# Kernel optimization log

Measured on AMD Instinct MI355X. Metric: run time of the kernel, lower is better.

Reference implementation:

```python
import jax, jax.numpy as jnp
import numpy as np

EMBED = 512
HEADS = 8
FMUL = 4
TAU = 2.0
V_TH = 1.0      # spiking threshold (spikingjelly default)
ALPHA = 2.0     # ATan surrogate alpha (spikingjelly default)
EPS = 1e-5


@jax.custom_vjp
def spike_fn(v):
    # Heaviside spike with ATan surrogate gradient (spikingjelly surrogate.ATan)
    return (v >= V_TH).astype(v.dtype)

def _spike_fwd(v):
    return spike_fn(v), v

def _spike_bwd(v, g):
    t = (jnp.pi / 2.0) * ALPHA * (v - V_TH)
    return (g * (ALPHA / 2.0) / (1.0 + t * t),)

spike_fn.defvjp(_spike_fwd, _spike_bwd)


def layernorm(x, g, b):
    mu = jnp.mean(x, axis=-1, keepdims=True)
    var = jnp.mean(jnp.square(x - mu), axis=-1, keepdims=True)
    return (x - mu) * jax.lax.rsqrt(var + EPS) * g + b


def setup_inputs() -> dict:
    key = jax.random.key(0)
    ks = jax.random.split(key, 12)
    m, s, e = 4, 2048, EMBED
    f = e * FMUL
    sc = 0.02
    return {
        "x":  jax.random.normal(ks[0], (m, s, e), jnp.float32),
        "wq": jax.random.normal(ks[1], (e, e), jnp.float32) * sc,
        "bq": jnp.zeros((e,), jnp.float32),
        "wk": jax.random.normal(ks[2], (e, e), jnp.float32) * sc,
        "bk": jnp.zeros((e,), jnp.float32),
        "wv": jax.random.normal(ks[3], (e, e), jnp.float32) * sc,
        "bv": jnp.zeros((e,), jnp.float32),
        "w1": jax.random.normal(ks[4], (e, f), jnp.float32) * sc,
        "b1": jnp.zeros((f,), jnp.float32),
        "w2": jax.random.normal(ks[5], (f, e), jnp.float32) * sc,
        "b2": jnp.zeros((e,), jnp.float32),
        "g1": jnp.ones((e,), jnp.float32),
        "be1": jnp.zeros((e,), jnp.float32),
        "g2": jnp.ones((e,), jnp.float32),
        "be2": jnp.zeros((e,), jnp.float32),
    }


def reference(x, wq, bq, wk, bk, wv, bv, w1, b1, w2, b2, g1, be1, g2, be2):
    m, s, e = x.shape
    h = HEADS
    d = e // h

    # --- pre-norm attention (NOTE: original has NO 1/sqrt(d) scaling) ---
    n1 = layernorm(x, g1, be1)
    q = (n1 @ wq + bq).reshape(m, s, h, d).transpose(0, 2, 1, 3)  # [m,h,s,d]
    k = (n1 @ wk + bk).reshape(m, s, h, d).transpose(0, 2, 1, 3)
    v = (n1 @ wv + bv).reshape(m, s, h, d).transpose(0, 2, 1, 3)
    scores = jnp.einsum('bhqd,bhkd->bhqk', q, k)       # [m,h,s,s], unscaled
    attn = jax.nn.softmax(scores, axis=-1)
    ctx = jnp.einsum('bhqk,bhkd->bhqd', attn, v)       # [m,h,s,d]
    att_out = ctx.transpose(0, 2, 1, 3).reshape(m, s, e)

    x = x + att_out
    # dropout p=0.4 is identity at inference (eval path in the original)

    # --- FFN with spiking activation ---
    n2 = layernorm(x, g2, be2)
    h1 = n2 @ w1 + b1                                  # [m,s,4e]
    # single-step LIF charge from v=0: v = v + (x - v)/tau = x/tau
    spikes = spike_fn(h1 / TAU)
    return x + (spikes @ w2 + b2)
```

## Files before the change

kernel.cpp:

```cpp
#include <hip/hip_runtime.h>
#include <stdint.h>

#define EMB 512
#define SEQ 2048
#define MB 4
#define NH 8
#define HD 64
#define ROWS (MB*SEQ)
#define MARGIN 0.02f
#define CAP 65536
#define LOG2E 1.44269504f
#define EXPB (-17.3123405f)

typedef unsigned short u16;
typedef __attribute__((ext_vector_type(8))) short bf16x8;
typedef __attribute__((ext_vector_type(4))) float f32x4;
typedef __attribute__((ext_vector_type(2))) unsigned int u32x2;
typedef __attribute__((ext_vector_type(4))) unsigned int u32x4;

union Frag { u32x2 u[2]; bf16x8 v; };
union Frag4 { unsigned u[4]; bf16x8 v; };

__device__ __forceinline__ u16 f2bf(float f) {
  union { float f; unsigned u; } a; a.f = f;
  unsigned r = a.u + 0x7FFFu + ((a.u >> 16) & 1u);
  return (u16)(r >> 16);
}
__device__ __forceinline__ float bflo(unsigned u) {
  union { unsigned u; float f; } c; c.u = u << 16; return c.f;
}
__device__ __forceinline__ float bfhi(unsigned u) {
  union { unsigned u; float f; } c; c.u = u & 0xffff0000u; return c.f;
}
__device__ __forceinline__ void gld16(const void* g, void* l) {
  __builtin_amdgcn_global_load_lds(
      (const __attribute__((address_space(1))) void*)g,
      (__attribute__((address_space(3))) void*)l, 16, 0, 0);
}


__global__ __launch_bounds__(256) void k_prep(
    const float* __restrict__ x, const float* __restrict__ g1, const float* __restrict__ be1,
    const float* __restrict__ wq, const float* __restrict__ wk,
    const float* __restrict__ wv, const float* __restrict__ w1,
    u16* __restrict__ n1, u16* __restrict__ wqkvT, u16* __restrict__ w1T,
    int* __restrict__ cnt) {
  __shared__ float tile[32][33];
  int b = blockIdx.x, tid = threadIdx.x;
  if (b < 1792) {
    const float* src; u16* dst; int N, bx, by;
    if (b < 768) {
      int z = b >> 8, rem = b & 255; bx = rem & 15; by = rem >> 4; N = 512;
      src = (z == 0) ? wq : ((z == 1) ? wk : wv);
      dst = wqkvT + z * 512 * 512;
    } else {
      int rem = b - 768; bx = rem & 63; by = rem >> 6; N = 2048;
      src = w1; dst = w1T;
    }
    int tx = tid & 31, ty = tid >> 5;
    int k0 = by * 32, n0 = bx * 32;
    for (int i = 0; i < 32; i += 8)
      tile[ty + i][tx] = src[(size_t)(k0 + ty + i) * N + n0 + tx];
    __syncthreads();
    for (int i = 0; i < 32; i += 8)
      dst[(size_t)(n0 + ty + i) * 512 + k0 + tx] = f2bf(tile[tx][ty + i]);
  } else {
    if (b == 1792 && tid < 2) cnt[tid] = 0;
    int wid = tid >> 6, lane = tid & 63;
    int row = (b - 1792) * 4 + wid;
    const float* xr = x + (size_t)row * EMB + lane * 8;
    f32x4 v0 = *(const f32x4*)xr;
    f32x4 v1 = *(const f32x4*)(xr + 4);
    float s = v0.x+v0.y+v0.z+v0.w + v1.x+v1.y+v1.z+v1.w;
    float q = v0.x*v0.x+v0.y*v0.y+v0.z*v0.z+v0.w*v0.w
            + v1.x*v1.x+v1.y*v1.y+v1.z*v1.z+v1.w*v1.w;
    #pragma unroll
    for (int o = 1; o < 64; o <<= 1) { s += __shfl_xor(s, o); q += __shfl_xor(q, o); }
    float mu = s * (1.0f/512.0f);
    float rs = 1.0f / sqrtf(q * (1.0f/512.0f) - mu*mu + 1e-5f);
    f32x4 ga = *(const f32x4*)(g1 + lane*8), gb = *(const f32x4*)(g1 + lane*8 + 4);
    f32x4 ba = *(const f32x4*)(be1 + lane*8), bb = *(const f32x4*)(be1 + lane*8 + 4);
    union { u16 h[8]; u32x4 v; } o8;
    o8.h[0] = f2bf((v0.x-mu)*rs*ga.x + ba.x); o8.h[1] = f2bf((v0.y-mu)*rs*ga.y + ba.y);
    o8.h[2] = f2bf((v0.z-mu)*rs*ga.z + ba.z); o8.h[3] = f2bf((v0.w-mu)*rs*ga.w + ba.w);
    o8.h[4] = f2bf((v1.x-mu)*rs*gb.x + bb.x); o8.h[5] = f2bf((v1.y-mu)*rs*gb.y + bb.y);
    o8.h[6] = f2bf((v1.z-mu)*rs*gb.z + bb.z); o8.h[7] = f2bf((v1.w-mu)*rs*gb.w + bb.w);
    *(u32x4*)(n1 + (size_t)row * EMB + lane * 8) = o8.v;
  }
}

__global__ __launch_bounds__(256) void k_ln2(const float* __restrict__ x,
    const u16* __restrict__ att, const float* __restrict__ g, const float* __restrict__ b,
    const float* __restrict__ b2, float* __restrict__ x2, u16* __restrict__ n2,
    float* __restrict__ out) {
  int wid = threadIdx.x >> 6, lane = threadIdx.x & 63;
  int row = blockIdx.x * 4 + wid;
  size_t base = (size_t)row * EMB + lane * 8;
  u32x4 av = *(const u32x4*)(att + base);
  f32x4 t0, t1;
  t0.x = bflo(av.x); t0.y = bfhi(av.x); t0.z = bflo(av.y); t0.w = bfhi(av.y);
  t1.x = bflo(av.z); t1.y = bfhi(av.z); t1.z = bflo(av.w); t1.w = bfhi(av.w);
  f32x4 v0 = *(const f32x4*)(x + base)     + t0;
  f32x4 v1 = *(const f32x4*)(x + base + 4) + t1;
  *(f32x4*)(x2 + base) = v0;
  *(f32x4*)(x2 + base + 4) = v1;
  *(f32x4*)(out + base)     = v0 + *(const f32x4*)(b2 + lane*8);
  *(f32x4*)(out + base + 4) = v1 + *(const f32x4*)(b2 + lane*8 + 4);
  float s = v0.x+v0.y+v0.z+v0.w + v1.x+v1.y+v1.z+v1.w;
  float q = v0.x*v0.x+v0.y*v0.y+v0.z*v0.z+v0.w*v0.w
          + v1.x*v1.x+v1.y*v1.y+v1.z*v1.z+v1.w*v1.w;
  #pragma unroll
  for (int o = 1; o < 64; o <<= 1) { s += __shfl_xor(s, o); q += __shfl_xor(q, o); }
  float mu = s * (1.0f/512.0f);
  float rs = 1.0f / sqrtf(q * (1.0f/512.0f) - mu*mu + 1e-5f);
  f32x4 ga = *(const f32x4*)(g + lane*8), gb = *(const f32x4*)(g + lane*8 + 4);
  f32x4 ba = *(const f32x4*)(b + lane*8), bb = *(const f32x4*)(b + lane*8 + 4);
  union { u16 h[8]; u32x4 v; } o8;
  o8.h[0] = f2bf((v0.x-mu)*rs*ga.x + ba.x); o8.h[1] = f2bf((v0.y-mu)*rs*ga.y + ba.y);
  o8.h[2] = f2bf((v0.z-mu)*rs*ga.z + ba.z); o8.h[3] = f2bf((v0.w-mu)*rs*ga.w + ba.w);
  o8.h[4] = f2bf((v1.x-mu)*rs*gb.x + bb.x); o8.h[5] = f2bf((v1.y-mu)*rs*gb.y + bb.y);
  o8.h[6] = f2bf((v1.z-mu)*rs*gb.z + bb.z); o8.h[7] = f2bf((v1.w-mu)*rs*gb.w + bb.w);
  *(u32x4*)(n2 + (size_t)row * EMB + lane * 8) = o8.v;
}

#define GEMM_CORE(A_, Bt_, m0_, n0_)                                           \
  __shared__ u16 As[2][128 * 32];                                              \
  __shared__ u16 Bs[2][128 * 32];                                              \
  int tid = threadIdx.x;                                                       \
  int wid = tid >> 6, lane = tid & 63;                                         \
  int quad = lane >> 4, ln15 = lane & 15;                                      \
  int wm = (wid >> 1) * 64, wn = (wid & 1) * 64;                               \
  int arow = lane >> 2, acol = (lane & 3) * 8;                                 \
  const u16* gA0 = A_  + (size_t)(m0_ + wid * 32 + arow) * 512 + acol;         \
  const u16* gA1 = gA0 + (size_t)16 * 512;                                     \
  const u16* gB0 = Bt_ + (size_t)(n0_ + wid * 32 + arow) * 512 + acol;         \
  const u16* gB1 = gB0 + (size_t)16 * 512;                                     \
  f32x4 acc[4][4] = {};                                                        \
  gld16(gA0, &As[0][(wid * 32) * 32]); gld16(gA1, &As[0][(wid * 32 + 16) * 32]);\
  gld16(gB0, &Bs[0][(wid * 32) * 32]); gld16(gB1, &Bs[0][(wid * 32 + 16) * 32]);\
  for (int kt = 0; kt < 16; kt++) {                                            \
    int cur = kt & 1;                                                          \
    __syncthreads();                                                           \
    if (kt < 15) {                                                             \
      int ko = (kt + 1) * 32;                                                  \
      gld16(gA0 + ko, &As[cur ^ 1][(wid * 32) * 32]);                          \
      gld16(gA1 + ko, &As[cur ^ 1][(wid * 32 + 16) * 32]);                     \
      gld16(gB0 + ko, &Bs[cur ^ 1][(wid * 32) * 32]);                          \
      gld16(gB1 + ko, &Bs[cur ^ 1][(wid * 32 + 16) * 32]);                     \
    }                                                                          \
    bf16x8 af[4], bf[4];                                                       \
    _Pragma("unroll")                                                          \
    for (int i = 0; i < 4; i++) {                                              \
      af[i] = *(const bf16x8*)&As[cur][(wm + i * 16 + ln15) * 32 + quad * 8];  \
      bf[i] = *(const bf16x8*)&Bs[cur][(wn + i * 16 + ln15) * 32 + quad * 8];  \
    }                                                                          \
    _Pragma("unroll")                                                          \
    for (int i = 0; i < 4; i++)                                                \
      _Pragma("unroll")                                                        \
      for (int j = 0; j < 4; j++)                                              \
        acc[i][j] = __builtin_amdgcn_mfma_f32_16x16x32_bf16(af[i], bf[j],      \
                                                            acc[i][j], 0, 0, 0);\
  }                                                                            \
  __syncthreads();

__global__ __launch_bounds__(256) void k_gemm_qkv(
    const u16* __restrict__ A, const u16* __restrict__ Bt,
    const float* __restrict__ bq, const float* __restrict__ bk, const float* __restrict__ bv,
    u16* __restrict__ Qb, u16* __restrict__ Kb, u16* __restrict__ Vtb) {
  int m0 = blockIdx.y * 128, n0 = blockIdx.x * 128;
  GEMM_CORE(A, Bt, m0, n0)
  #pragma unroll
  for (int j = 0; j < 4; j++) {
    int n = n0 + wn + j * 16 + ln15;
    int t = n >> 9, cc = n & 511, head = cc >> 6, dd = cc & 63;
    float bias = (t == 0) ? bq[cc] : ((t == 1) ? bk[cc] : bv[cc]);
    #pragma unroll
    for (int i = 0; i < 4; i++) {
      int row0 = m0 + wm + i * 16 + quad * 4;
      int mm = row0 >> 11, ss0 = row0 & 2047;
      if (t == 2) {
        union { u16 h[4]; u32x2 v; } pk;
        #pragma unroll
        for (int r = 0; r < 4; r++) pk.h[r] = f2bf(acc[i][j][r] + bias);
        *(u32x2*)(Vtb + ((size_t)(mm * 8 + head) * 64 + dd) * 2048 + ss0) = pk.v;
      } else {
        u16* dst = (t == 0) ? Qb : Kb;
        #pragma unroll
        for (int r = 0; r < 4; r++)
          dst[((size_t)(mm * 8 + head) * 2048 + ss0 + r) * 64 + dd] =
              f2bf(acc[i][j][r] + bias);
      }
    }
  }
}

__global__ __launch_bounds__(256) void k_gemm_ffn1(
    const u16* __restrict__ A, const u16* __restrict__ Bt, const float* __restrict__ b1,
    int* __restrict__ cnt, unsigned* __restrict__ spikeL, unsigned* __restrict__ candL) {
  int m0 = blockIdx.y * 128, n0 = blockIdx.x * 128;
  GEMM_CORE(A, Bt, m0, n0)
  #pragma unroll
  for (int j = 0; j < 4; j++) {
    int n = n0 + wn + j * 16 + ln15;
    float bias = b1[n];
    #pragma unroll
    for (int i = 0; i < 4; i++) {
      #pragma unroll
      for (int r = 0; r < 4; r++) {
        int row = m0 + wm + i * 16 + quad * 4 + r;
        float hv = acc[i][j][r] + bias;
        if (hv >= 2.0f - MARGIN) {
          if (hv >= 2.0f + MARGIN) {
            int ix = atomicAdd(&cnt[0], 1);
            if (ix < CAP) spikeL[ix] = (unsigned)(row * 2048 + n);
          } else {
            int ix = atomicAdd(&cnt[1], 1);
            if (ix < CAP) candL[ix] = (unsigned)(row * 2048 + n);
          }
        }
      }
    }
  }
}

#define F_STAGE(BUF, T0)                                                       \
  do {                                                                         \
    gld16(gK0 + (size_t)(T0)       * 4096, &L.SB[BUF][0][0][rb0 * 64]);        \
    gld16(gK1 + (size_t)(T0)       * 4096, &L.SB[BUF][0][0][rb1 * 64]);        \
    gld16(gK0 + (size_t)((T0) + 1) * 4096, &L.SB[BUF][0][1][rb0 * 64]);        \
    gld16(gK1 + (size_t)((T0) + 1) * 4096, &L.SB[BUF][0][1][rb1 * 64]);        \
    gld16(gV0 + (T0) * 64,       &L.SB[BUF][1][0][rb0 * 64]);                  \
    gld16(gV1 + (T0) * 64,       &L.SB[BUF][1][0][rb1 * 64]);                  \
    gld16(gV0 + ((T0) + 1) * 64, &L.SB[BUF][1][1][rb0 * 64]);                  \
    gld16(gV1 + ((T0) + 1) * 64, &L.SB[BUF][1][1][rb1 * 64]);                  \
  } while (0)

#define F_INNER(BUF, SUB)                                                      \
  do {                                                                         \
    const u16* Kc = L.SB[BUF][0][SUB];                                         \
    const u16* Vc = L.SB[BUF][1][SUB];                                         \
    f32x4 s4[2][4];                                                            \
    _Pragma("unroll")                                                          \
    for (int j = 0; j < 4; j++) {                                              \
      bf16x8 a = *(const bf16x8*)(Kc + (j * 16 + ln15) * 64 + ((quad ^ lm) * 8)); \
      s4[0][j] = __builtin_amdgcn_mfma_f32_16x16x32_bf16(a, aQ[0][0].v, z4, 0, 0, 0); \
      s4[1][j] = __builtin_amdgcn_mfma_f32_16x16x32_bf16(a, aQ[1][0].v, z4, 0, 0, 0); \
    }                                                                          \
    _Pragma("unroll")                                                          \
    for (int j = 0; j < 4; j++) {                                              \
      bf16x8 a = *(const bf16x8*)(Kc + (j * 16 + ln15) * 64 + (((4 + quad) ^ lm) * 8)); \
      s4[0][j] = __builtin_amdgcn_mfma_f32_16x16x32_bf16(a, aQ[0][1].v, s4[0][j], 0, 0, 0); \
      s4[1][j] = __builtin_amdgcn_mfma_f32_16x16x32_bf16(a, aQ[1][1].v, s4[1][j], 0, 0, 0); \
    }                                                                          \
    Frag4 bP[2][2];                                                            \
    _Pragma("unroll")                                                          \
    for (int h = 0; h < 2; h++) {                                              \
      unsigned pr[4][4];                                                       \
      _Pragma("unroll")                                                        \
      for (int j = 0; j < 4; j++)                                              \
        _Pragma("unroll")                                                      \
        for (int r = 0; r < 4; r++) {                                          \
          float p = __builtin_amdgcn_exp2f(fmaf(s4[h][j][r], LOG2E, EXPB));    \
          l[h] += p;                                                           \
          union { float f; unsigned u; } cc; cc.f = p;                         \
          pr[j][r] = cc.u;                                                     \
        }                                                                      \
      _Pragma("unroll")                                                        \
      for (int t = 0; t < 2; t++) {                                            \
        bP[h][t].u[0] = __builtin_amdgcn_perm(pr[2*t][1],   pr[2*t][0],   0x07060302u); \
        bP[h][t].u[1] = __builtin_amdgcn_perm(pr[2*t][3],   pr[2*t][2],   0x07060302u); \
        bP[h][t].u[2] = __builtin_amdgcn_perm(pr[2*t+1][1], pr[2*t+1][0], 0x07060302u); \
        bP[h][t].u[3] = __builtin_amdgcn_perm(pr[2*t+1][3], pr[2*t+1][2], 0x07060302u); \
      }                                                                        \
    }                                                                          \
    _Pragma("unroll")                                                          \
    for (int t = 0; t < 2; t++)                                                \
      _Pragma("unroll")                                                        \
      for (int j = 0; j < 4; j++) {                                            \
        int row = j * 16 + ln15;                                               \
        int c0 = 4 * t + (quad >> 1), sub = (quad & 1) * 4;                    \
        Frag aV;                                                               \
        aV.u[0] = *(const u32x2*)(Vc + row * 64 + ((c0 ^ lm) * 8) + sub);      \
        aV.u[1] = *(const u32x2*)(Vc + row * 64 + (((c0 + 2) ^ lm) * 8) + sub);\
        U[0][j] = __builtin_amdgcn_mfma_f32_16x16x32_bf16(aV.v, bP[0][t].v,    \
                                                          U[0][j], 0, 0, 0);   \
        U[1][j] = __builtin_amdgcn_mfma_f32_16x16x32_bf16(aV.v, bP[1][t].v,    \
                                                          U[1][j], 0, 0, 0);   \
      }                                                                        \
  } while (0)

#define F_STEP(CUR, S)                                                         \
  do {                                                                         \
    __syncthreads();                                                           \
    if ((S) < 15) F_STAGE((CUR) ^ 1, 2 * (S) + 2);                             \
    F_INNER(CUR, 0);                                                           \
    F_INNER(CUR, 1);                                                           \
  } while (0)

__global__ __launch_bounds__(256, 2) void k_flash(
    const u16* __restrict__ Q, const u16* __restrict__ K,
    const u16* __restrict__ Vt, u16* __restrict__ att) {
  __shared__ union {
    u16 SB[2][2][2][64 * 64];
    float T[4][16 * 68];
  } L;
  int tid = threadIdx.x, wid = tid >> 6, lane = tid & 63;
  int quad = lane >> 4, ln15 = lane & 15, lm = ln15 & 7;
  int qb = blockIdx.x, head = blockIdx.y, mm = blockIdx.z;
  int mh = mm * 8 + head;
  const u16* Qp = Q  + (size_t)mh * SEQ * HD;
  const u16* Kp = K  + (size_t)mh * SEQ * HD;
  const u16* Vp = Vt + (size_t)mh * HD * SEQ;
  int q0 = qb * 128 + wid * 32;

  Frag aQ[2][2];
  #pragma unroll
  for (int h = 0; h < 2; h++)
    #pragma unroll
    for (int t = 0; t < 2; t++) {
      u32x4 g = *(const u32x4*)(Qp + (size_t)(q0 + h * 16 + ln15) * 64 + t * 32 + quad * 8);
      aQ[h][t].u[0].x = g.x; aQ[h][t].u[0].y = g.y;
      aQ[h][t].u[1].x = g.z; aQ[h][t].u[1].y = g.w;
    }
  const f32x4 z4 = {0.f, 0.f, 0.f, 0.f};

  int srow = lane >> 3;
  int sch  = (lane & 7) ^ (srow & 7);
  int rb0 = wid * 16, rb1 = wid * 16 + 8;
  const u16* gK0 = Kp + (size_t)(rb0 + srow) * 64 + sch * 8;
  const u16* gK1 = Kp + (size_t)(rb1 + srow) * 64 + sch * 8;
  const u16* gV0 = Vp + (size_t)(rb0 + srow) * SEQ + sch * 8;
  const u16* gV1 = Vp + (size_t)(rb1 + srow) * SEQ + sch * 8;

  float l[2] = {0.f, 0.f};
  f32x4 U[2][4] = {};

  F_STAGE(0, 0);
  for (int it = 0; it < 8; it++) {
    F_STEP(0, 2 * it);
    F_STEP(1, 2 * it + 1);
  }
  __syncthreads();

  #pragma unroll
  for (int h = 0; h < 2; h++) {
    float lv = l[h];
    lv += __shfl_xor(lv, 16);
    lv += __shfl_xor(lv, 32);
    float rl = 1.0f / lv;
    float* Tw = L.T[wid];
    #pragma unroll
    for (int j = 0; j < 4; j++)
      *(f32x4*)(Tw + ln15 * 68 + j * 16 + quad * 4) = U[h][j] * rl;
    #pragma unroll
    for (int s = 0; s < 4; s++) {
      f32x4 o = *(const f32x4*)(Tw + (quad * 4 + s) * 68 + ln15 * 4);
      union { u16 h4[4]; u32x2 v; } pk;
      pk.h4[0] = f2bf(o.x); pk.h4[1] = f2bf(o.y);
      pk.h4[2] = f2bf(o.z); pk.h4[3] = f2bf(o.w);
      *(u32x2*)(att + ((size_t)mm * SEQ + q0 + h * 16 + quad * 4 + s) * EMB +
                head * 64 + ln15 * 4) = pk.v;
    }
  }
}

__global__ __launch_bounds__(256) void k_fixup(
    const float* __restrict__ x2, const float* __restrict__ w1, const float* __restrict__ b1,
    const float* __restrict__ g2, const float* __restrict__ be2,
    int* __restrict__ cnt, unsigned* __restrict__ spikeL, const unsigned* __restrict__ candL) {
  __shared__ float sb[8];
  int tid = threadIdx.x;
  int nC = cnt[1]; if (nC > CAP) nC = CAP;
  for (int e = blockIdx.x; e < nC; e += gridDim.x) {
    unsigned v = candL[e];
    int row = (int)(v >> 11), col = (int)(v & 2047u);
    const float* xr = x2 + (size_t)row * 512;
    float x0 = xr[tid], x1 = xr[tid + 256];
    float s = x0 + x1, q = x0 * x0 + x1 * x1;
    #pragma unroll
    for (int o = 1; o < 64; o <<= 1) { s += __shfl_xor(s, o); q += __shfl_xor(q, o); }
    if ((tid & 63) == 0) { sb[tid >> 6] = s; sb[4 + (tid >> 6)] = q; }
    __syncthreads();
    float st = sb[0] + sb[1] + sb[2] + sb[3];
    float qt = sb[4] + sb[5] + sb[6] + sb[7];
    __syncthreads();
    float mu = st * (1.f / 512.f);
    float rs = 1.f / sqrtf(qt * (1.f / 512.f) - mu * mu + 1e-5f);
    float na = (x0 - mu) * rs * g2[tid] + be2[tid];
    float nb = (x1 - mu) * rs * g2[tid + 256] + be2[tid + 256];
    float dd = na * w1[(size_t)tid * 2048 + col] + nb * w1[(size_t)(tid + 256) * 2048 + col];
    #pragma unroll
    for (int o = 1; o < 64; o <<= 1) dd += __shfl_xor(dd, o);
    if ((tid & 63) == 0) sb[tid >> 6] = dd;
    __syncthreads();
    if (tid == 0) {
      float hv = sb[0] + sb[1] + sb[2] + sb[3] + b1[col];
      if (hv >= 2.0f) { int ix = atomicAdd(&cnt[0], 1); if (ix < CAP) spikeL[ix] = v; }
    }
    __syncthreads();
  }
}

__global__ void k_apply(const float* __restrict__ w2, const int* __restrict__ cnt,
                        const unsigned* __restrict__ spikeL, float* __restrict__ out) {
  int n = cnt[0]; if (n > CAP) n = CAP;
  int tid = threadIdx.x;
  for (int e = blockIdx.x; e < n; e += gridDim.x) {
    unsigned v = spikeL[e];
    int row = (int)(v >> 11), col = (int)(v & 2047u);
    atomicAdd(&out[(size_t)row * 512 + tid * 2 + 0], w2[(size_t)col * 512 + tid * 2 + 0]);
    atomicAdd(&out[(size_t)row * 512 + tid * 2 + 1], w2[(size_t)col * 512 + tid * 2 + 1]);
  }
}


extern "C" void kernel_launch(void* const* d_in, const int* in_sizes, int n_in,
                              void* d_out, int out_size, void* d_ws, size_t ws_size,
                              hipStream_t stream) {
  (void)in_sizes; (void)n_in; (void)out_size; (void)ws_size;
  const float* x   = (const float*)d_in[0];
  const float* wq  = (const float*)d_in[1];
  const float* bq  = (const float*)d_in[2];
  const float* wk  = (const float*)d_in[3];
  const float* bk  = (const float*)d_in[4];
  const float* wv  = (const float*)d_in[5];
  const float* bv  = (const float*)d_in[6];
  const float* w1  = (const float*)d_in[7];
  const float* b1  = (const float*)d_in[8];
  const float* w2  = (const float*)d_in[9];
  const float* b2  = (const float*)d_in[10];
  const float* g1  = (const float*)d_in[11];
  const float* be1 = (const float*)d_in[12];
  const float* g2  = (const float*)d_in[13];
  const float* be2 = (const float*)d_in[14];
  float* out = (float*)d_out;

  char* w = (char*)d_ws;
  size_t off = 0;
  auto take = [&](size_t bytes) { char* p = w + off; off += (bytes + 255) & ~(size_t)255; return p; };
  int*      cnt    = (int*)take(256);
  u16*      n1     = (u16*)take((size_t)ROWS * EMB * 2);
  u16*      wqkvT  = (u16*)take((size_t)1536 * 512 * 2);
  u16*      w1T    = (u16*)take((size_t)2048 * 512 * 2);
  u16*      Qb     = (u16*)take((size_t)MB * NH * SEQ * HD * 2);
  u16*      Kb     = (u16*)take((size_t)MB * NH * SEQ * HD * 2);
  u16*      Vtb    = (u16*)take((size_t)MB * NH * SEQ * HD * 2);
  u16*      att    = (u16*)take((size_t)ROWS * EMB * 2);
  float*    x2     = (float*)take((size_t)ROWS * EMB * 4);
  u16*      n2     = (u16*)take((size_t)ROWS * EMB * 2);
  unsigned* spikeL = (unsigned*)take((size_t)CAP * 4);
  unsigned* candL  = (unsigned*)take((size_t)CAP * 4);

  k_prep<<<3840, 256, 0, stream>>>(x, g1, be1, wq, wk, wv, w1, n1, wqkvT, w1T, cnt);
  k_gemm_qkv<<<dim3(12, 64), 256, 0, stream>>>(n1, wqkvT, bq, bk, bv, Qb, Kb, Vtb);
  k_flash<<<dim3(16, 8, 4), 256, 0, stream>>>(Qb, Kb, Vtb, att);
  k_ln2<<<ROWS / 4, 256, 0, stream>>>(x, att, g2, be2, b2, x2, n2, out);
  k_gemm_ffn1<<<dim3(16, 64), 256, 0, stream>>>(n2, w1T, b1, cnt, spikeL, candL);
  k_fixup<<<256, 256, 0, stream>>>(x2, w1, b1, g2, be2, cnt, spikeL, candL);
  k_apply<<<128, 256, 0, stream>>>(w2, cnt, spikeL, out);
}
```

Baseline: 208.7 us.

## Halve flash query tile per wave, raise occupancy, add MFMA priority hints

Each wave in the flash attention kernel now handles 16 query rows instead of 32, and the grid doubles to 32 query blocks per head. Shared staging shrinks to one 64-key tile per buffer, and launch bounds go from 2 to 4 blocks per CU, trading register reuse of K/V fragments for occupancy and latency hiding. s_setprio hints are wrapped around the MFMA sections so one wave's MFMAs overlap other waves' exp work. The risk is that each K/V tile is now loaded by twice as many blocks, with more barriers per unit of compute.

```diff
diff --git a/kernel.cpp b/kernel.cpp
--- a/kernel.cpp
+++ b/kernel.cpp
@@ -225,54 +225,48 @@
 
 #define F_STAGE(BUF, T0)                                                       \
   do {                                                                         \
-    gld16(gK0 + (size_t)(T0)       * 4096, &L.SB[BUF][0][0][rb0 * 64]);        \
-    gld16(gK1 + (size_t)(T0)       * 4096, &L.SB[BUF][0][0][rb1 * 64]);        \
-    gld16(gK0 + (size_t)((T0) + 1) * 4096, &L.SB[BUF][0][1][rb0 * 64]);        \
-    gld16(gK1 + (size_t)((T0) + 1) * 4096, &L.SB[BUF][0][1][rb1 * 64]);        \
-    gld16(gV0 + (T0) * 64,       &L.SB[BUF][1][0][rb0 * 64]);                  \
-    gld16(gV1 + (T0) * 64,       &L.SB[BUF][1][0][rb1 * 64]);                  \
-    gld16(gV0 + ((T0) + 1) * 64, &L.SB[BUF][1][1][rb0 * 64]);                  \
-    gld16(gV1 + ((T0) + 1) * 64, &L.SB[BUF][1][1][rb1 * 64]);                  \
+    gld16(gK0 + (size_t)(T0) * 4096, &L.SB[BUF][0][rb0 * 64]);                 \
+    gld16(gK1 + (size_t)(T0) * 4096, &L.SB[BUF][0][rb1 * 64]);                 \
+    gld16(gV0 + (T0) * 64, &L.SB[BUF][1][rb0 * 64]);                           \
+    gld16(gV1 + (T0) * 64, &L.SB[BUF][1][rb1 * 64]);                           \
   } while (0)
 
-#define F_INNER(BUF, SUB)                                                      \
+#define F_INNER(BUF)                                                           \
   do {                                                                         \
-    const u16* Kc = L.SB[BUF][0][SUB];                                         \
-    const u16* Vc = L.SB[BUF][1][SUB];                                         \
-    f32x4 s4[2][4];                                                            \
+    const u16* Kc = L.SB[BUF][0];                                              \
+    const u16* Vc = L.SB[BUF][1];                                              \
+    f32x4 s4[4];                                                               \
+    __builtin_amdgcn_s_setprio(1);                                             \
     _Pragma("unroll")                                                          \
     for (int j = 0; j < 4; j++) {                                              \
       bf16x8 a = *(const bf16x8*)(Kc + (j * 16 + ln15) * 64 + ((quad ^ lm) * 8)); \
-      s4[0][j] = __builtin_amdgcn_mfma_f32_16x16x32_bf16(a, aQ[0][0].v, z4, 0, 0, 0); \
-      s4[1][j] = __builtin_amdgcn_mfma_f32_16x16x32_bf16(a, aQ[1][0].v, z4, 0, 0, 0); \
+      s4[j] = __builtin_amdgcn_mfma_f32_16x16x32_bf16(a, aQ[0].v, z4, 0, 0, 0);\
     }                                                                          \
     _Pragma("unroll")                                                          \
     for (int j = 0; j < 4; j++) {                                              \
       bf16x8 a = *(const bf16x8*)(Kc + (j * 16 + ln15) * 64 + (((4 + quad) ^ lm) * 8)); \
-      s4[0][j] = __builtin_amdgcn_mfma_f32_16x16x32_bf16(a, aQ[0][1].v, s4[0][j], 0, 0, 0); \
-      s4[1][j] = __builtin_amdgcn_mfma_f32_16x16x32_bf16(a, aQ[1][1].v, s4[1][j], 0, 0, 0); \
+      s4[j] = __builtin_amdgcn_mfma_f32_16x16x32_bf16(a, aQ[1].v, s4[j], 0, 0, 0); \
     }                                                                          \
-    Frag4 bP[2][2];                                                            \
-    _Pragma("unroll")                                                          \
-    for (int h = 0; h < 2; h++) {                                              \
-      unsigned pr[4][4];                                                       \
+    __builtin_amdgcn_s_setprio(0);                                             \
+    Frag4 bP[2];                                                               \
+    unsigned pr[4][4];                                                         \
+    _Pragma("unroll")                                                          \
+    for (int j = 0; j < 4; j++)                                                \
       _Pragma("unroll")                                                        \
-      for (int j = 0; j < 4; j++)                                              \
-        _Pragma("unroll")                                                      \
-        for (int r = 0; r < 4; r++) {                                          \
-          float p = __builtin_amdgcn_exp2f(fmaf(s4[h][j][r], LOG2E, EXPB));    \
-          l[h] += p;                                                           \
-          union { float f; unsigned u; } cc; cc.f = p;                         \
-          pr[j][r] = cc.u;                                                     \
-        }                                                                      \
-      _Pragma("unroll")                                                        \
-      for (int t = 0; t < 2; t++) {                                            \
-        bP[h][t].u[0] = __builtin_amdgcn_perm(pr[2*t][1],   pr[2*t][0],   0x07060302u); \
-        bP[h][t].u[1] = __builtin_amdgcn_perm(pr[2*t][3],   pr[2*t][2],   0x07060302u); \
-        bP[h][t].u[2] = __builtin_amdgcn_perm(pr[2*t+1][1], pr[2*t+1][0], 0x07060302u); \
-        bP[h][t].u[3] = __builtin_amdgcn_perm(pr[2*t+1][3], pr[2*t+1][2], 0x07060302u); \
+      for (int r = 0; r < 4; r++) {                                            \
+        float p = __builtin_amdgcn_exp2f(fmaf(s4[j][r], LOG2E, EXPB));         \
+        l4[r] += p;                                                            \
+        union { float f; unsigned u; } cc; cc.f = p;                           \
+        pr[j][r] = cc.u;                                                       \
       }                                                                        \
+    _Pragma("unroll")                                                          \
+    for (int t = 0; t < 2; t++) {                                              \
+      bP[t].u[0] = __builtin_amdgcn_perm(pr[2*t][1],   pr[2*t][0],   0x07060302u); \
+      bP[t].u[1] = __builtin_amdgcn_perm(pr[2*t][3],   pr[2*t][2],   0x07060302u); \
+      bP[t].u[2] = __builtin_amdgcn_perm(pr[2*t+1][1], pr[2*t+1][0], 0x07060302u); \
+      bP[t].u[3] = __builtin_amdgcn_perm(pr[2*t+1][3], pr[2*t+1][2], 0x07060302u); \
     }                                                                          \
+    __builtin_amdgcn_s_setprio(1);                                             \
     _Pragma("unroll")                                                          \
     for (int t = 0; t < 2; t++)                                                \
       _Pragma("unroll")                                                        \
@@ -282,26 +276,17 @@
         Frag aV;                                                               \
         aV.u[0] = *(const u32x2*)(Vc + row * 64 + ((c0 ^ lm) * 8) + sub);      \
         aV.u[1] = *(const u32x2*)(Vc + row * 64 + (((c0 + 2) ^ lm) * 8) + sub);\
-        U[0][j] = __builtin_amdgcn_mfma_f32_16x16x32_bf16(aV.v, bP[0][t].v,    \
-                                                          U[0][j], 0, 0, 0);   \
-        U[1][j] = __builtin_amdgcn_mfma_f32_16x16x32_bf16(aV.v, bP[1][t].v,    \
-                                                          U[1][j], 0, 0, 0);   \
+        U[j] = __builtin_amdgcn_mfma_f32_16x16x32_bf16(aV.v, bP[t].v,          \
+                                                       U[j], 0, 0, 0);         \
       }                                                                        \
+    __builtin_amdgcn_s_setprio(0);                                             \
   } while (0)
 
-#define F_STEP(CUR, S)                                                         \
-  do {                                                                         \
-    __syncthreads();                                                           \
-    if ((S) < 15) F_STAGE((CUR) ^ 1, 2 * (S) + 2);                             \
-    F_INNER(CUR, 0);                                                           \
-    F_INNER(CUR, 1);                                                           \
-  } while (0)
-
-__global__ __launch_bounds__(256, 2) void k_flash(
+__global__ __launch_bounds__(256, 4) void k_flash(
     const u16* __restrict__ Q, const u16* __restrict__ K,
     const u16* __restrict__ Vt, u16* __restrict__ att) {
   __shared__ union {
-    u16 SB[2][2][2][64 * 64];
+    u16 SB[2][2][64 * 64];
     float T[4][16 * 68];
   } L;
   int tid = threadIdx.x, wid = tid >> 6, lane = tid & 63;
@@ -311,17 +296,15 @@
   const u16* Qp = Q  + (size_t)mh * SEQ * HD;
   const u16* Kp = K  + (size_t)mh * SEQ * HD;
   const u16* Vp = Vt + (size_t)mh * HD * SEQ;
-  int q0 = qb * 128 + wid * 32;
-
-  Frag aQ[2][2];
-  #pragma unroll
-  for (int h = 0; h < 2; h++)
-    #pragma unroll
-    for (int t = 0; t < 2; t++) {
-      u32x4 g = *(const u32x4*)(Qp + (size_t)(q0 + h * 16 + ln15) * 64 + t * 32 + quad * 8);
-      aQ[h][t].u[0].x = g.x; aQ[h][t].u[0].y = g.y;
-      aQ[h][t].u[1].x = g.z; aQ[h][t].u[1].y = g.w;
-    }
+  int q0 = qb * 64 + wid * 16;
+
+  Frag aQ[2];
+  #pragma unroll
+  for (int t = 0; t < 2; t++) {
+    u32x4 g = *(const u32x4*)(Qp + (size_t)(q0 + ln15) * 64 + t * 32 + quad * 8);
+    aQ[t].u[0].x = g.x; aQ[t].u[0].y = g.y;
+    aQ[t].u[1].x = g.z; aQ[t].u[1].y = g.w;
+  }
   const f32x4 z4 = {0.f, 0.f, 0.f, 0.f};
 
   int srow = lane >> 3;
@@ -332,35 +315,36 @@
   const u16* gV0 = Vp + (size_t)(rb0 + srow) * SEQ + sch * 8;
   const u16* gV1 = Vp + (size_t)(rb1 + srow) * SEQ + sch * 8;
 
-  float l[2] = {0.f, 0.f};
-  f32x4 U[2][4] = {};
+  f32x4 l4 = {0.f, 0.f, 0.f, 0.f};
+  f32x4 U[4] = {};
 
   F_STAGE(0, 0);
-  for (int it = 0; it < 8; it++) {
-    F_STEP(0, 2 * it);
-    F_STEP(1, 2 * it + 1);
+  for (int it = 0; it < 16; it++) {
+    __syncthreads();
+    F_STAGE(1, 2 * it + 1);
+    F_INNER(0);
+    __syncthreads();
+    if (it < 15) F_STAGE(0, 2 * it + 2);
+    F_INNER(1);
   }
   __syncthreads();
 
-  #pragma unroll
-  for (int h = 0; h < 2; h++) {
-    float lv = l[h];
-    lv += __shfl_xor(lv, 16);
-    lv += __shfl_xor(lv, 32);
-    float rl = 1.0f / lv;
-    float* Tw = L.T[wid];
-    #pragma unroll
-    for (int j = 0; j < 4; j++)
-      *(f32x4*)(Tw + ln15 * 68 + j * 16 + quad * 4) = U[h][j] * rl;
-    #pragma unroll
-    for (int s = 0; s < 4; s++) {
-      f32x4 o = *(const f32x4*)(Tw + (quad * 4 + s) * 68 + ln15 * 4);
-      union { u16 h4[4]; u32x2 v; } pk;
-      pk.h4[0] = f2bf(o.x); pk.h4[1] = f2bf(o.y);
-      pk.h4[2] = f2bf(o.z); pk.h4[3] = f2bf(o.w);
-      *(u32x2*)(att + ((size_t)mm * SEQ + q0 + h * 16 + quad * 4 + s) * EMB +
-                head * 64 + ln15 * 4) = pk.v;
-    }
+  float lv = l4.x + l4.y + l4.z + l4.w;
+  lv += __shfl_xor(lv, 16);
+  lv += __shfl_xor(lv, 32);
+  float rl = 1.0f / lv;
+  float* Tw = L.T[wid];
+  #pragma unroll
+  for (int j = 0; j < 4; j++)
+    *(f32x4*)(Tw + ln15 * 68 + j * 16 + quad * 4) = U[j] * rl;
+  #pragma unroll
+  for (int s = 0; s < 4; s++) {
+    f32x4 o = *(const f32x4*)(Tw + (quad * 4 + s) * 68 + ln15 * 4);
+    union { u16 h4[4]; u32x2 v; } pk;
+    pk.h4[0] = f2bf(o.x); pk.h4[1] = f2bf(o.y);
+    pk.h4[2] = f2bf(o.z); pk.h4[3] = f2bf(o.w);
+    *(u32x2*)(att + ((size_t)mm * SEQ + q0 + quad * 4 + s) * EMB +
+              head * 64 + ln15 * 4) = pk.v;
   }
 }
 
@@ -453,7 +437,7 @@
 
   k_prep<<<3840, 256, 0, stream>>>(x, g1, be1, wq, wk, wv, w1, n1, wqkvT, w1T, cnt);
   k_gemm_qkv<<<dim3(12, 64), 256, 0, stream>>>(n1, wqkvT, bq, bk, bv, Qb, Kb, Vtb);
-  k_flash<<<dim3(16, 8, 4), 256, 0, stream>>>(Qb, Kb, Vtb, att);
+  k_flash<<<dim3(32, 8, 4), 256, 0, stream>>>(Qb, Kb, Vtb, att);
   k_ln2<<<ROWS / 4, 256, 0, stream>>>(x, att, g2, be2, b2, x2, n2, out);
   k_gemm_ffn1<<<dim3(16, 64), 256, 0, stream>>>(n2, w1T, b1, cnt, spikeL, candL);
   k_fixup<<<256, 256, 0, stream>>>(x2, w1, b1, g2, be2, cnt, spikeL, candL);
```

New measurement: 219.7 us. +5.3%, slower.

## Shrink flash-attention blocks to two waves, add setprio around MFMA phases

Applied to the files above, without the earlier changes.

The flash attention kernel now runs 128-thread blocks covering 64 queries each, launching twice as many blocks, with half the shared memory per block. The double-buffered stages are restructured to a single 64-key tile per buffer, synchronised twice per iteration. s_setprio raises wave priority during the MFMA phases, and the row-sum accumulator is split into four lanes to shorten the dependency chain. The aim is better occupancy and overlap across waves, at the cost of more barriers and more K/V reloads per query.

```diff
diff --git a/kernel.cpp b/kernel.cpp
--- a/kernel.cpp
+++ b/kernel.cpp
@@ -225,21 +225,22 @@
 
 #define F_STAGE(BUF, T0)                                                       \
   do {                                                                         \
-    gld16(gK0 + (size_t)(T0)       * 4096, &L.SB[BUF][0][0][rb0 * 64]);        \
-    gld16(gK1 + (size_t)(T0)       * 4096, &L.SB[BUF][0][0][rb1 * 64]);        \
-    gld16(gK0 + (size_t)((T0) + 1) * 4096, &L.SB[BUF][0][1][rb0 * 64]);        \
-    gld16(gK1 + (size_t)((T0) + 1) * 4096, &L.SB[BUF][0][1][rb1 * 64]);        \
-    gld16(gV0 + (T0) * 64,       &L.SB[BUF][1][0][rb0 * 64]);                  \
-    gld16(gV1 + (T0) * 64,       &L.SB[BUF][1][0][rb1 * 64]);                  \
-    gld16(gV0 + ((T0) + 1) * 64, &L.SB[BUF][1][1][rb0 * 64]);                  \
-    gld16(gV1 + ((T0) + 1) * 64, &L.SB[BUF][1][1][rb1 * 64]);                  \
+    gld16(gK0 + (size_t)(T0) * 4096, &L.SB[BUF][0][(rb +  0) * 64]);           \
+    gld16(gK1 + (size_t)(T0) * 4096, &L.SB[BUF][0][(rb +  8) * 64]);           \
+    gld16(gK2 + (size_t)(T0) * 4096, &L.SB[BUF][0][(rb + 16) * 64]);           \
+    gld16(gK3 + (size_t)(T0) * 4096, &L.SB[BUF][0][(rb + 24) * 64]);           \
+    gld16(gV0 + (T0) * 64, &L.SB[BUF][1][(rb +  0) * 64]);                     \
+    gld16(gV1 + (T0) * 64, &L.SB[BUF][1][(rb +  8) * 64]);                     \
+    gld16(gV2 + (T0) * 64, &L.SB[BUF][1][(rb + 16) * 64]);                     \
+    gld16(gV3 + (T0) * 64, &L.SB[BUF][1][(rb + 24) * 64]);                     \
   } while (0)
 
-#define F_INNER(BUF, SUB)                                                      \
+#define F_INNER(BUF)                                                           \
   do {                                                                         \
-    const u16* Kc = L.SB[BUF][0][SUB];                                         \
-    const u16* Vc = L.SB[BUF][1][SUB];                                         \
+    const u16* Kc = L.SB[BUF][0];                                              \
+    const u16* Vc = L.SB[BUF][1];                                              \
     f32x4 s4[2][4];                                                            \
+    __builtin_amdgcn_s_setprio(1);                                             \
     _Pragma("unroll")                                                          \
     for (int j = 0; j < 4; j++) {                                              \
       bf16x8 a = *(const bf16x8*)(Kc + (j * 16 + ln15) * 64 + ((quad ^ lm) * 8)); \
@@ -252,6 +253,7 @@
       s4[0][j] = __builtin_amdgcn_mfma_f32_16x16x32_bf16(a, aQ[0][1].v, s4[0][j], 0, 0, 0); \
       s4[1][j] = __builtin_amdgcn_mfma_f32_16x16x32_bf16(a, aQ[1][1].v, s4[1][j], 0, 0, 0); \
     }                                                                          \
+    __builtin_amdgcn_s_setprio(0);                                             \
     Frag4 bP[2][2];                                                            \
     _Pragma("unroll")                                                          \
     for (int h = 0; h < 2; h++) {                                              \
@@ -261,7 +263,7 @@
         _Pragma("unroll")                                                      \
         for (int r = 0; r < 4; r++) {                                          \
           float p = __builtin_amdgcn_exp2f(fmaf(s4[h][j][r], LOG2E, EXPB));    \
-          l[h] += p;                                                           \
+          l4[h][r] += p;                                                       \
           union { float f; unsigned u; } cc; cc.f = p;                         \
           pr[j][r] = cc.u;                                                     \
         }                                                                      \
@@ -273,6 +275,7 @@
         bP[h][t].u[3] = __builtin_amdgcn_perm(pr[2*t+1][3], pr[2*t+1][2], 0x07060302u); \
       }                                                                        \
     }                                                                          \
+    __builtin_amdgcn_s_setprio(1);                                             \
     _Pragma("unroll")                                                          \
     for (int t = 0; t < 2; t++)                                                \
       _Pragma("unroll")                                                        \
@@ -287,22 +290,15 @@
         U[1][j] = __builtin_amdgcn_mfma_f32_16x16x32_bf16(aV.v, bP[1][t].v,    \
                                                           U[1][j], 0, 0, 0);   \
       }                                                                        \
+    __builtin_amdgcn_s_setprio(0);                                             \
   } while (0)
 
-#define F_STEP(CUR, S)                                                         \
-  do {                                                                         \
-    __syncthreads();                                                           \
-    if ((S) < 15) F_STAGE((CUR) ^ 1, 2 * (S) + 2);                             \
-    F_INNER(CUR, 0);                                                           \
-    F_INNER(CUR, 1);                                                           \
-  } while (0)
-
-__global__ __launch_bounds__(256, 2) void k_flash(
+__global__ __launch_bounds__(128, 4) void k_flash(
     const u16* __restrict__ Q, const u16* __restrict__ K,
     const u16* __restrict__ Vt, u16* __restrict__ att) {
   __shared__ union {
-    u16 SB[2][2][2][64 * 64];
-    float T[4][16 * 68];
+    u16 SB[2][2][64 * 64];
+    float T[2][16 * 68];
   } L;
   int tid = threadIdx.x, wid = tid >> 6, lane = tid & 63;
   int quad = lane >> 4, ln15 = lane & 15, lm = ln15 & 7;
@@ -311,7 +307,7 @@
   const u16* Qp = Q  + (size_t)mh * SEQ * HD;
   const u16* Kp = K  + (size_t)mh * SEQ * HD;
   const u16* Vp = Vt + (size_t)mh * HD * SEQ;
-  int q0 = qb * 128 + wid * 32;
+  int q0 = qb * 64 + wid * 32;
 
   Frag aQ[2][2];
   #pragma unroll
@@ -326,25 +322,33 @@
 
   int srow = lane >> 3;
   int sch  = (lane & 7) ^ (srow & 7);
-  int rb0 = wid * 16, rb1 = wid * 16 + 8;
-  const u16* gK0 = Kp + (size_t)(rb0 + srow) * 64 + sch * 8;
-  const u16* gK1 = Kp + (size_t)(rb1 + srow) * 64 + sch * 8;
-  const u16* gV0 = Vp + (size_t)(rb0 + srow) * SEQ + sch * 8;
-  const u16* gV1 = Vp + (size_t)(rb1 + srow) * SEQ + sch * 8;
-
-  float l[2] = {0.f, 0.f};
+  int rb = wid * 32;
+  const u16* gK0 = Kp + (size_t)(rb +  0 + srow) * 64 + sch * 8;
+  const u16* gK1 = Kp + (size_t)(rb +  8 + srow) * 64 + sch * 8;
+  const u16* gK2 = Kp + (size_t)(rb + 16 + srow) * 64 + sch * 8;
+  const u16* gK3 = Kp + (size_t)(rb + 24 + srow) * 64 + sch * 8;
+  const u16* gV0 = Vp + (size_t)(rb +  0 + srow) * SEQ + sch * 8;
+  const u16* gV1 = Vp + (size_t)(rb +  8 + srow) * SEQ + sch * 8;
+  const u16* gV2 = Vp + (size_t)(rb + 16 + srow) * SEQ + sch * 8;
+  const u16* gV3 = Vp + (size_t)(rb + 24 + srow) * SEQ + sch * 8;
+
+  f32x4 l4[2] = {{0.f,0.f,0.f,0.f}, {0.f,0.f,0.f,0.f}};
   f32x4 U[2][4] = {};
 
   F_STAGE(0, 0);
-  for (int it = 0; it < 8; it++) {
-    F_STEP(0, 2 * it);
-    F_STEP(1, 2 * it + 1);
+  for (int it = 0; it < 16; it++) {
+    __syncthreads();
+    F_STAGE(1, 2 * it + 1);
+    F_INNER(0);
+    __syncthreads();
+    if (it < 15) F_STAGE(0, 2 * it + 2);
+    F_INNER(1);
   }
   __syncthreads();
 
   #pragma unroll
   for (int h = 0; h < 2; h++) {
-    float lv = l[h];
+    float lv = l4[h].x + l4[h].y + l4[h].z + l4[h].w;
     lv += __shfl_xor(lv, 16);
     lv += __shfl_xor(lv, 32);
     float rl = 1.0f / lv;
@@ -453,7 +457,7 @@
 
   k_prep<<<3840, 256, 0, stream>>>(x, g1, be1, wq, wk, wv, w1, n1, wqkvT, w1T, cnt);
   k_gemm_qkv<<<dim3(12, 64), 256, 0, stream>>>(n1, wqkvT, bq, bk, bv, Qb, Kb, Vtb);
-  k_flash<<<dim3(16, 8, 4), 256, 0, stream>>>(Qb, Kb, Vtb, att);
+  k_flash<<<dim3(32, 8, 4), 128, 0, stream>>>(Qb, Kb, Vtb, att);
   k_ln2<<<ROWS / 4, 256, 0, stream>>>(x, att, g2, be2, b2, x2, n2, out);
   k_gemm_ffn1<<<dim3(16, 64), 256, 0, stream>>>(n2, w1T, b1, cnt, spikeL, candL);
   k_fixup<<<256, 256, 0, stream>>>(x2, w1, b1, g2, be2, cnt, spikeL, candL);
```

Result: slower. 218.0 us (+4.5%).
